# Performance work log

Measured on AMD Instinct MI355X. Metric: run time of the kernel, lower is better.

Reference implementation:

```python
import jax, jax.numpy as jnp
import numpy as np

GRID = (192, 96, 192)
NUM_MATERIALS = 8
WORLD_SCALE = 2.0
OCC_THRESHOLD = 0.01
TEMPERATURE = 1.0


def _look_at(eye, target, up):
    eye = np.asarray(eye, np.float32); target = np.asarray(target, np.float32); up = np.asarray(up, np.float32)
    f = target - eye; f = f / np.linalg.norm(f)
    r = np.cross(f, up); r = r / np.linalg.norm(r)
    u = np.cross(r, f)
    view = np.eye(4, dtype=np.float32)
    view[0, :3] = r;  view[0, 3] = -r @ eye
    view[1, :3] = u;  view[1, 3] = -u @ eye
    view[2, :3] = -f; view[2, 3] = f @ eye
    return view


def _perspective(fov_deg, aspect, near, far):
    f = 1.0 / np.tan(np.radians(fov_deg) / 2.0)
    p = np.zeros((4, 4), dtype=np.float32)
    p[0, 0] = f / aspect
    p[1, 1] = f
    p[2, 2] = (far + near) / (near - far)
    p[2, 3] = 2.0 * far * near / (near - far)
    p[3, 2] = -1.0
    return p


def setup_inputs() -> dict:
    key = jax.random.key(0)
    k1, k2 = jax.random.split(key)
    X, Y, Z = GRID
    occupancy_logits = jax.random.normal(k1, (X, Y, Z), dtype=jnp.float32)
    material_logits = jax.random.normal(k2, (X, Y, Z, NUM_MATERIALS), dtype=jnp.float32)
    # grid world extent: x,z in [-X/2, X/2]*scale, y in [0, Y]*scale
    camera_view = jnp.asarray(_look_at(eye=(0.0, 250.0, 700.0), target=(0.0, 96.0, 0.0), up=(0.0, 1.0, 0.0)))
    camera_proj = jnp.asarray(_perspective(60.0, 1.0, 0.1, 2000.0))
    return {
        'occupancy_logits': occupancy_logits,
        'material_logits': material_logits,
        'camera_view': camera_view,
        'camera_proj': camera_proj,
        'max_blocks': 100000,
    }


def _voxel_centers(X, Y, Z):
    # centers = (idx + 0.5 + offset) * world_scale, offset = (-X/2, 0, -Z/2)
    cx = (jnp.arange(X, dtype=jnp.float32) + 0.5 - X / 2.0) * WORLD_SCALE
    cy = (jnp.arange(Y, dtype=jnp.float32) + 0.5) * WORLD_SCALE
    cz = (jnp.arange(Z, dtype=jnp.float32) + 0.5 - Z / 2.0) * WORLD_SCALE
    gx, gy, gz = jnp.meshgrid(cx, cy, cz, indexing='ij')
    return jnp.stack([gx.ravel(), gy.ravel(), gz.ravel()], axis=-1)  # (N, 3)


def reference(occupancy_logits, material_logits, camera_view, camera_proj, max_blocks):
    X, Y, Z = occupancy_logits.shape
    N = X * Y * Z
    occ = jax.nn.sigmoid(occupancy_logits).reshape(-1)          # (N,)
    active = occ > OCC_THRESHOLD                                # torch.nonzero -> mask

    centers = _voxel_centers(X, Y, Z)                           # (N, 3) world centers

    # frustum test in NDC (world_to_clip with combined MVP)
    mvp = camera_proj @ camera_view                             # (4, 4)
    clip = centers @ mvp[:, :3].T + mvp[:, 3]                   # (N, 4)
    w = jnp.maximum(clip[:, 3], 1e-6)
    ndc = clip[:, :3] / w[:, None]
    visible = jnp.all((ndc >= -1.0) & (ndc <= 1.0), axis=-1)

    valid = active & visible

    # depth-based top-k: keep max_blocks nearest valid voxels
    view_z = centers @ camera_view[2, :3] + camera_view[2, 3]
    depth = jnp.maximum(-view_z, 0.0)
    score = jnp.where(valid, -depth, -jnp.inf)                  # nearest first
    _, idx = jax.lax.top_k(score, max_blocks)
    keep = jnp.zeros((N,), dtype=bool).at[idx].set(valid[idx])  # pruned_mask scatter

    pruned_weights = jnp.where(keep, occ, 0.0).reshape(X, Y, Z)

    # render prep: per-voxel material distribution scaled by occupancy weight
    mat_probs = jax.nn.softmax(material_logits / TEMPERATURE, axis=-1)
    return pruned_weights[..., None] * mat_probs                # (X, Y, Z, M)
```

## Files before the change

kernel.cpp:

```cpp
#include <hip/hip_runtime.h>

#define GX 192
#define GY 96
#define GZ 192
#define GRP (GY*GZ)
#define NVOX (GX*GRP)

#define NXC 12
#define XCW (GX/NXC)
#define GBLK (GRP/256)

#define K2T 1024
#define GPT (GRP/K2T)
#define WBINS 4096
#define BPT (WBINS/K2T)

#define WS_MVP    0
#define WS_G16    64
#define WS_DEPTH  (WS_G16 + GRP*16)
#define WS_SEL    (WS_DEPTH + GRP*4)
#define WS_TLIST  (WS_SEL + 16)
#define WS_TPREF  (WS_TLIST + 1024)
#define WS_NTIED  (WS_TPREF + GX*4)

typedef float f4 __attribute__((ext_vector_type(4)));

#define BSUM(w) (((w) & 255u) + (((w) >> 8) & 255u) + (((w) >> 16) & 255u) + ((w) >> 24))

__device__ __forceinline__ bool voxel_valid(int x, int g,
                                            const float* __restrict__ occL,
                                            const float* M,
                                            float* occ_out)
{
    int y = g / GZ;
    int z = g - y * GZ;
    float cx = (float)(2 * x - 191);
    float cy = (float)(2 * y + 1);
    float cz = (float)(2 * z - 191);

    float logit = occL[(size_t)x * GRP + g];
    float occ = 1.0f / (1.0f + expf(-logit));
    *occ_out = occ;
    if (!(occ > 0.01f)) return false;

    float c0 = __fadd_rn(__fmaf_rn(cz, M[2],  __fmaf_rn(cy, M[1],  __fmul_rn(cx, M[0]))),  M[3]);
    float c1 = __fadd_rn(__fmaf_rn(cz, M[6],  __fmaf_rn(cy, M[5],  __fmul_rn(cx, M[4]))),  M[7]);
    float c2 = __fadd_rn(__fmaf_rn(cz, M[10], __fmaf_rn(cy, M[9],  __fmul_rn(cx, M[8]))),  M[11]);
    float c3 = __fadd_rn(__fmaf_rn(cz, M[14], __fmaf_rn(cy, M[13], __fmul_rn(cx, M[12]))), M[15]);

    float w  = fmaxf(c3, 1e-6f);
    float nx = c0 / w;
    float ny = c1 / w;
    float nz = c2 / w;
    return (nx >= -1.0f) && (nx <= 1.0f) &&
           (ny >= -1.0f) && (ny <= 1.0f) &&
           (nz >= -1.0f) && (nz <= 1.0f);
}

__device__ __forceinline__ void compute_mvp_lds(const float* view, const float* proj,
                                                float* s_mvp, int tid)
{
    if (tid < 16) {
        int r = tid >> 2, c = tid & 3;
        float acc = 0.0f;
        for (int k = 0; k < 4; ++k)
            acc = __fadd_rn(acc, __fmul_rn(proj[r * 4 + k], view[k * 4 + c]));
        s_mvp[tid] = acc;
    }
}

__device__ __forceinline__ unsigned wave_incl_scan(unsigned v, int lane)
{
    #pragma unroll
    for (int off = 1; off < 64; off <<= 1) {
        unsigned u = (unsigned)__shfl_up((int)v, off);
        if (lane >= off) v += u;
    }
    return v;
}

__global__ __launch_bounds__(256) void k_prep_count(
    const float* __restrict__ view, const float* __restrict__ proj,
    const float* __restrict__ occL,
    float* __restrict__ mvpOut,
    unsigned char* __restrict__ g16,
    unsigned* __restrict__ depthBits)
{
    __shared__ float s_mvp[16];
    int tid = threadIdx.x;
    compute_mvp_lds(view, proj, s_mvp, tid);
    __syncthreads();

    int b  = blockIdx.x;
    int gb = b % GBLK;
    int xc = b / GBLK;
    int g  = gb * 256 + tid;

    if (b == 0 && tid < 16) mvpOut[tid] = s_mvp[tid];

    if (xc == 0) {
        int y = g / GZ;
        int z = g - y * GZ;
        float cy = (float)(2 * y + 1);
        float cz = (float)(2 * z - 191);
        float seed = __fmul_rn(-191.0f, view[8]);
        float vz = __fadd_rn(__fmaf_rn(cz, view[10], __fmaf_rn(cy, view[9], seed)), view[11]);
        float d  = fmaxf(-vz, 0.0f);
        unsigned db = __float_as_uint(d);
        __builtin_nontemporal_store(db, (unsigned*)(g16 + (size_t)g * 16));
        __builtin_nontemporal_store(db, &depthBits[g]);
    }

    unsigned c = 0;
    int x0 = xc * XCW;
    #pragma unroll
    for (int j = 0; j < XCW; ++j) {
        float occ;
        if (voxel_valid(x0 + j, g, occL, s_mvp, &occ)) ++c;
    }
    __builtin_nontemporal_store((unsigned char)c, g16 + (size_t)g * 16 + 4 + xc);
}

__global__ __launch_bounds__(1024) void k_select(
    const float* __restrict__ view, const float* __restrict__ proj,
    const float* __restrict__ occL,
    const unsigned char* __restrict__ g16,
    const int* __restrict__ maxBlocksPtr,
    unsigned* __restrict__ sel,
    unsigned* __restrict__ tiedList,
    unsigned* __restrict__ tiedPrefX,
    unsigned* __restrict__ nTiedG)
{
    __shared__ float s_mvp[16];
    __shared__ unsigned s_h[WBINS];
    __shared__ unsigned s_w[16];
    __shared__ unsigned s_wT[16], s_wMn[16], s_wMx[16];
    __shared__ unsigned s_tot, s_mn, s_mx, s_chTot;
    __shared__ unsigned s_found, s_prefix, s_remK;
    __shared__ unsigned s_list[256];
    __shared__ int s_n;
    __shared__ unsigned s_cntX[GX];

    int tid  = threadIdx.x;
    int lane = tid & 63;
    int wid  = tid >> 6;
    compute_mvp_lds(view, proj, s_mvp, tid);

    uint4 q[GPT];
    #pragma unroll
    for (int k = 0; k < GPT; ++k)
        q[k] = *(const uint4*)(g16 + (size_t)(tid + k * K2T) * 16);

    unsigned d[GPT], c[GPT];
    #pragma unroll
    for (int k = 0; k < GPT; ++k) {
        d[k] = q[k].x;
        c[k] = BSUM(q[k].y) + BSUM(q[k].z) + BSUM(q[k].w);
    }

    unsigned tot = 0, mn = 0xFFFFFFFFu, mx = 0;
    #pragma unroll
    for (int k = 0; k < GPT; ++k) {
        tot += c[k];
        if (c[k]) {
            unsigned hi = d[k] >> 16;
            mn = min(mn, hi);
            mx = max(mx, hi);
        }
    }
    for (int m = 1; m < 64; m <<= 1) {
        tot += (unsigned)__shfl_xor((int)tot, m);
        mn = min(mn, (unsigned)__shfl_xor((int)mn, m));
        mx = max(mx, (unsigned)__shfl_xor((int)mx, m));
    }
    if (lane == 0) { s_wT[wid] = tot; s_wMn[wid] = mn; s_wMx[wid] = mx; }
    __syncthreads();
    if (tid == 0) {
        unsigned t2 = 0, m2 = 0xFFFFFFFFu, x2 = 0;
        for (int w = 0; w < 16; ++w) {
            t2 += s_wT[w]; m2 = min(m2, s_wMn[w]); x2 = max(x2, s_wMx[w]);
        }
        s_tot = t2; s_mn = m2; s_mx = x2;
        s_found = 0;
    }
    __syncthreads();
    unsigned K = (unsigned)maxBlocksPtr[0];
    tot = s_tot; mn = s_mn; mx = s_mx;

    if (tot <= K) {
        if (tid == 0) {
            sel[0] = 0xFFFFFFFFu;
            sel[1] = 0x7FFFFFFFu;
            *nTiedG = 0u;
        }
        return;
    }

    unsigned remK = K;
    unsigned prefix = 0;
    unsigned span = mx - mn + 1u;
    unsigned nchunks = (span + WBINS - 1u) / WBINS;
    for (unsigned ch = 0; ch < nchunks; ++ch) {
        unsigned base = mn + ch * WBINS;
        #pragma unroll
        for (int j = 0; j < BPT; ++j) s_h[tid + j * K2T] = 0;
        __syncthreads();
        #pragma unroll
        for (int k = 0; k < GPT; ++k) {
            if (c[k]) {
                unsigned hi = d[k] >> 16;
                if (hi >= base && hi < base + WBINS)
                    atomicAdd(&s_h[hi - base], c[k]);
            }
        }
        __syncthreads();
        unsigned ps = 0;
        #pragma unroll
        for (int j = 0; j < BPT; ++j) ps += s_h[tid * BPT + j];
        unsigned iw = wave_incl_scan(ps, lane);
        if (lane == 63) s_w[wid] = iw;
        __syncthreads();
        if (wid == 0) {
            unsigned wv = (lane < 16) ? s_w[lane] : 0u;
            unsigned wiw = wave_incl_scan(wv, lane);
            if (lane < 16) s_w[lane] = wiw - wv;
            if (lane == 15) s_chTot = wiw;
        }
        __syncthreads();
        unsigned incl = iw + s_w[wid];
        unsigned chunkTot = s_chTot;
        unsigned excl = incl - ps;
        if (remK <= chunkTot && excl < remK && remK <= incl) {
            unsigned cum = excl;
            #pragma unroll
            for (int j = 0; j < BPT; ++j) {
                unsigned hv = s_h[tid * BPT + j];
                if (cum < remK && remK <= cum + hv) {
                    s_found  = 1u;
                    s_prefix = base + (unsigned)(tid * BPT + j);
                    s_remK   = remK - cum;
                }
                cum += hv;
            }
        }
        __syncthreads();
        if (s_found) { prefix = s_prefix; remK = s_remK; break; }
        remK -= chunkTot;
        __syncthreads();
    }

    for (int p = 0; p < 2; ++p) {
        int matchShift = (p == 0) ? 16 : 8;
        int digitShift = (p == 0) ? 8 : 0;
        if (tid < 256) s_h[tid] = 0;
        __syncthreads();
        #pragma unroll
        for (int k = 0; k < GPT; ++k) {
            if (c[k] && (d[k] >> matchShift) == prefix)
                atomicAdd(&s_h[(d[k] >> digitShift) & 255u], c[k]);
        }
        __syncthreads();
        unsigned ps = (tid < 256) ? s_h[tid] : 0u;
        unsigned iw = wave_incl_scan(ps, lane);
        if (lane == 63) s_w[wid] = iw;
        __syncthreads();
        if (wid == 0) {
            unsigned wv = (lane < 16) ? s_w[lane] : 0u;
            unsigned wiw = wave_incl_scan(wv, lane);
            if (lane < 16) s_w[lane] = wiw - wv;
        }
        __syncthreads();
        unsigned incl = iw + s_w[wid];
        unsigned excl = incl - ps;
        if (excl < remK && remK <= incl) {
            s_prefix = (prefix << 8) | (unsigned)tid;
            s_remK   = remK - excl;
        }
        __syncthreads();
        prefix = s_prefix; remK = s_remK;
        __syncthreads();
    }
    unsigned T = prefix;
    unsigned R = remK;

    if (tid == 0) s_n = 0;
    for (int x = tid; x < GX; x += K2T) s_cntX[x] = 0;
    __syncthreads();
    #pragma unroll
    for (int k = 0; k < GPT; ++k) {
        if (d[k] == T) {
            int idx = atomicAdd(&s_n, 1);
            if (idx < 256) s_list[idx] = (unsigned)(tid + k * K2T);
        }
    }
    __syncthreads();
    int n = min(s_n, 256);
    if (tid == 0) {
        for (int a = 1; a < n; ++a) {
            unsigned v = s_list[a];
            int b = a - 1;
            while (b >= 0 && s_list[b] > v) { s_list[b + 1] = s_list[b]; --b; }
            s_list[b + 1] = v;
        }
    }
    __syncthreads();
    int pairs = GX * n;
    for (int pr = tid; pr < pairs; pr += K2T) {
        int x = pr / n;
        int s = pr - x * n;
        float occ;
        if (voxel_valid(x, (int)s_list[s], occL, s_mvp, &occ))
            atomicAdd(&s_cntX[x], 1u);
    }
    __syncthreads();
    if (tid == 0) {
        unsigned run = 0;
        for (int x = 0; x < GX; ++x) { tiedPrefX[x] = run; run += s_cntX[x]; }
        *nTiedG = (unsigned)n;
        sel[0] = T;
        sel[1] = R;
    }
    if (tid < n) tiedList[tid] = s_list[tid];
}

__global__ __launch_bounds__(256) void k_out(
    const float* __restrict__ occL,
    const float* __restrict__ matL,
    const float* __restrict__ mvp,
    const unsigned* __restrict__ depthBits,
    const unsigned* __restrict__ sel,
    const unsigned* __restrict__ tiedList,
    const unsigned* __restrict__ tiedPrefX,
    const unsigned* __restrict__ nTiedPtr,
    float* __restrict__ out)
{
    int i = blockIdx.x * 256 + threadIdx.x;
    if (i >= NVOX) return;
    int x = i / GRP;
    int g = i - x * GRP;

    float occ;
    bool valid = voxel_valid(x, g, occL, mvp, &occ);
    bool keep = false;
    if (valid) {
        unsigned T  = sel[0];
        unsigned db = depthBits[g];
        if (db < T) {
            keep = true;
        } else if (db == T) {
            unsigned R = sel[1];
            unsigned rank = tiedPrefX[x];
            int n = (int)*nTiedPtr;
            for (int s = 0; s < n; ++s) {
                unsigned gs = tiedList[s];
                if (gs >= (unsigned)g) break;
                float o2;
                if (voxel_valid(x, (int)gs, occL, mvp, &o2)) ++rank;
            }
            keep = rank < R;
        }
    }

    f4 o0 = (f4)(0.0f);
    f4 o1 = (f4)(0.0f);
    if (keep) {
        const f4* mp = reinterpret_cast<const f4*>(matL) + (size_t)i * 2;
        f4 a = __builtin_nontemporal_load(mp);
        f4 b = __builtin_nontemporal_load(mp + 1);
        float mx = fmaxf(fmaxf(fmaxf(a[0], a[1]), fmaxf(a[2], a[3])),
                         fmaxf(fmaxf(b[0], b[1]), fmaxf(b[2], b[3])));
        float e0 = expf(a[0] - mx), e1 = expf(a[1] - mx), e2 = expf(a[2] - mx), e3 = expf(a[3] - mx);
        float e4 = expf(b[0] - mx), e5 = expf(b[1] - mx), e6 = expf(b[2] - mx), e7 = expf(b[3] - mx);
        float s = ((e0 + e1) + (e2 + e3)) + ((e4 + e5) + (e6 + e7));
        float inv = occ / s;
        o0[0] = e0 * inv; o0[1] = e1 * inv; o0[2] = e2 * inv; o0[3] = e3 * inv;
        o1[0] = e4 * inv; o1[1] = e5 * inv; o1[2] = e6 * inv; o1[3] = e7 * inv;
    }
    f4* op = reinterpret_cast<f4*>(out) + (size_t)i * 2;
    __builtin_nontemporal_store(o0, op);
    __builtin_nontemporal_store(o1, op + 1);
}

extern "C" void kernel_launch(void* const* d_in, const int* in_sizes, int n_in,
                              void* d_out, int out_size, void* d_ws, size_t ws_size,
                              hipStream_t stream)
{
    const float* occL = (const float*)d_in[0];
    const float* matL = (const float*)d_in[1];
    const float* view = (const float*)d_in[2];
    const float* proj = (const float*)d_in[3];
    const int*   mb   = (const int*)d_in[4];

    char* ws = (char*)d_ws;
    float*          mvp      = (float*)(ws + WS_MVP);
    unsigned char*  g16      = (unsigned char*)(ws + WS_G16);
    unsigned*       depthB   = (unsigned*)(ws + WS_DEPTH);
    unsigned*       sel      = (unsigned*)(ws + WS_SEL);
    unsigned*       tiedList = (unsigned*)(ws + WS_TLIST);
    unsigned*       tiedPref = (unsigned*)(ws + WS_TPREF);
    unsigned*       nTied    = (unsigned*)(ws + WS_NTIED);

    k_prep_count<<<NXC * GBLK, 256, 0, stream>>>(view, proj, occL, mvp, g16, depthB);
    k_select<<<1, K2T, 0, stream>>>(view, proj, occL, g16, mb,
                                    sel, tiedList, tiedPref, nTied);
    k_out<<<NVOX / 256, 256, 0, stream>>>(occL, matL, mvp, depthB, sel,
                                          tiedList, tiedPref, nTied, (float*)d_out);
}
```

Before: 66.79 us.

## Split selection into multi-block count reduction with last-block radix select

Replaces the single 1024-thread selection kernel with a 72-block kernel. Each block sums the per-group voxel counts into a byte array, and the last block to finish (detected with an atomic counter) runs a four-pass 8-bit radix select over recomputed depth bits. Dropping the wide chunked histogram is meant to shorten the serial single-block phase and spread the initial g16 reads across many CUs. In exchange the last block does 72 strided passes per radix round with only 256 threads, and a device-wide atomic plus threadfence handshake is added.

```diff
diff --git a/kernel.cpp b/kernel.cpp
--- a/kernel.cpp
+++ b/kernel.cpp
@@ -10,15 +10,15 @@
 #define XCW (GX/NXC)
 #define GBLK (GRP/256)
 
-#define K2T 1024
-#define GPT (GRP/K2T)
-#define WBINS 4096
-#define BPT (WBINS/K2T)
+#define SB   (GRP/256)
+#define SGPT (GRP/256)
 
 #define WS_MVP    0
 #define WS_G16    64
-#define WS_DEPTH  (WS_G16 + GRP*16)
-#define WS_SEL    (WS_DEPTH + GRP*4)
+#define WS_DEPTH  (WS_G16 + (size_t)GRP*16)
+#define WS_CSUM   (WS_DEPTH + GRP*4)
+#define WS_DONE   (WS_CSUM + GRP)
+#define WS_SEL    (WS_DONE + 16)
 #define WS_TLIST  (WS_SEL + 16)
 #define WS_TPREF  (WS_TLIST + 1024)
 #define WS_NTIED  (WS_TPREF + GX*4)
@@ -57,6 +57,18 @@
            (nz >= -1.0f) && (nz <= 1.0f);
 }
 
+__device__ __forceinline__ unsigned depth_bits(int g, float v8, float v9,
+                                               float v10, float v11)
+{
+    int y = g / GZ;
+    int z = g - y * GZ;
+    float cy = (float)(2 * y + 1);
+    float cz = (float)(2 * z - 191);
+    float seed = __fmul_rn(-191.0f, v8);
+    float vz = __fadd_rn(__fmaf_rn(cz, v10, __fmaf_rn(cy, v9, seed)), v11);
+    return __float_as_uint(fmaxf(-vz, 0.0f));
+}
+
 __device__ __forceinline__ void compute_mvp_lds(const float* view, const float* proj,
                                                 float* s_mvp, int tid)
 {
@@ -84,7 +96,8 @@
     const float* __restrict__ occL,
     float* __restrict__ mvpOut,
     unsigned char* __restrict__ g16,
-    unsigned* __restrict__ depthBits)
+    unsigned* __restrict__ depthBits,
+    unsigned* __restrict__ doneCnt)
 {
     __shared__ float s_mvp[16];
     int tid = threadIdx.x;
@@ -96,20 +109,13 @@
     int xc = b / GBLK;
     int g  = gb * 256 + tid;
 
-    if (b == 0 && tid < 16) mvpOut[tid] = s_mvp[tid];
-
-    if (xc == 0) {
-        int y = g / GZ;
-        int z = g - y * GZ;
-        float cy = (float)(2 * y + 1);
-        float cz = (float)(2 * z - 191);
-        float seed = __fmul_rn(-191.0f, view[8]);
-        float vz = __fadd_rn(__fmaf_rn(cz, view[10], __fmaf_rn(cy, view[9], seed)), view[11]);
-        float d  = fmaxf(-vz, 0.0f);
-        unsigned db = __float_as_uint(d);
-        __builtin_nontemporal_store(db, (unsigned*)(g16 + (size_t)g * 16));
-        __builtin_nontemporal_store(db, &depthBits[g]);
-    }
+    if (b == 0) {
+        if (tid < 16) mvpOut[tid] = s_mvp[tid];
+        if (tid == 0) *doneCnt = 0u;
+    }
+
+    if (xc == 0)
+        depthBits[g] = depth_bits(g, view[8], view[9], view[10], view[11]);
 
     unsigned c = 0;
     int x0 = xc * XCW;
@@ -118,160 +124,90 @@
         float occ;
         if (voxel_valid(x0 + j, g, occL, s_mvp, &occ)) ++c;
     }
-    __builtin_nontemporal_store((unsigned char)c, g16 + (size_t)g * 16 + 4 + xc);
-}
-
-__global__ __launch_bounds__(1024) void k_select(
+    g16[(size_t)g * 16 + 4 + xc] = (unsigned char)c;
+}
+
+__global__ __launch_bounds__(256) void k_sumsel(
     const float* __restrict__ view, const float* __restrict__ proj,
     const float* __restrict__ occL,
     const unsigned char* __restrict__ g16,
+    unsigned char* __restrict__ cnt8sum,
+    unsigned* __restrict__ doneCnt,
     const int* __restrict__ maxBlocksPtr,
     unsigned* __restrict__ sel,
     unsigned* __restrict__ tiedList,
     unsigned* __restrict__ tiedPrefX,
     unsigned* __restrict__ nTiedG)
 {
+    __shared__ unsigned s_last;
     __shared__ float s_mvp[16];
-    __shared__ unsigned s_h[WBINS];
-    __shared__ unsigned s_w[16];
-    __shared__ unsigned s_wT[16], s_wMn[16], s_wMx[16];
-    __shared__ unsigned s_tot, s_mn, s_mx, s_chTot;
-    __shared__ unsigned s_found, s_prefix, s_remK;
+    __shared__ unsigned s_h[256];
+    __shared__ unsigned s_w[4];
+    __shared__ unsigned s_tot;
+    __shared__ unsigned s_prefix, s_remK;
     __shared__ unsigned s_list[256];
     __shared__ int s_n;
     __shared__ unsigned s_cntX[GX];
 
-    int tid  = threadIdx.x;
+    int tid = threadIdx.x;
+    int g0  = blockIdx.x * 256 + tid;
+
+    uint4 q = *(const uint4*)(g16 + (size_t)g0 * 16);
+    cnt8sum[g0] = (unsigned char)(BSUM(q.y) + BSUM(q.z) + BSUM(q.w));
+
+    __threadfence();
+    if (tid == 0) {
+        unsigned old = atomicAdd(doneCnt, 1u);
+        s_last = (old == SB - 1) ? 1u : 0u;
+    }
+    __syncthreads();
+    if (!s_last) return;
+    __threadfence();
+
+    compute_mvp_lds(view, proj, s_mvp, tid);
+    float v8 = view[8], v9 = view[9], v10 = view[10], v11 = view[11];
     int lane = tid & 63;
     int wid  = tid >> 6;
-    compute_mvp_lds(view, proj, s_mvp, tid);
-
-    uint4 q[GPT];
-    #pragma unroll
-    for (int k = 0; k < GPT; ++k)
-        q[k] = *(const uint4*)(g16 + (size_t)(tid + k * K2T) * 16);
-
-    unsigned d[GPT], c[GPT];
-    #pragma unroll
-    for (int k = 0; k < GPT; ++k) {
-        d[k] = q[k].x;
-        c[k] = BSUM(q[k].y) + BSUM(q[k].z) + BSUM(q[k].w);
-    }
-
-    unsigned tot = 0, mn = 0xFFFFFFFFu, mx = 0;
-    #pragma unroll
-    for (int k = 0; k < GPT; ++k) {
-        tot += c[k];
-        if (c[k]) {
-            unsigned hi = d[k] >> 16;
-            mn = min(mn, hi);
-            mx = max(mx, hi);
-        }
-    }
-    for (int m = 1; m < 64; m <<= 1) {
-        tot += (unsigned)__shfl_xor((int)tot, m);
-        mn = min(mn, (unsigned)__shfl_xor((int)mn, m));
-        mx = max(mx, (unsigned)__shfl_xor((int)mx, m));
-    }
-    if (lane == 0) { s_wT[wid] = tot; s_wMn[wid] = mn; s_wMx[wid] = mx; }
-    __syncthreads();
-    if (tid == 0) {
-        unsigned t2 = 0, m2 = 0xFFFFFFFFu, x2 = 0;
-        for (int w = 0; w < 16; ++w) {
-            t2 += s_wT[w]; m2 = min(m2, s_wMn[w]); x2 = max(x2, s_wMx[w]);
-        }
-        s_tot = t2; s_mn = m2; s_mx = x2;
-        s_found = 0;
-    }
-    __syncthreads();
     unsigned K = (unsigned)maxBlocksPtr[0];
-    tot = s_tot; mn = s_mn; mx = s_mx;
-
-    if (tot <= K) {
-        if (tid == 0) {
-            sel[0] = 0xFFFFFFFFu;
-            sel[1] = 0x7FFFFFFFu;
-            *nTiedG = 0u;
-        }
-        return;
-    }
-
-    unsigned remK = K;
-    unsigned prefix = 0;
-    unsigned span = mx - mn + 1u;
-    unsigned nchunks = (span + WBINS - 1u) / WBINS;
-    for (unsigned ch = 0; ch < nchunks; ++ch) {
-        unsigned base = mn + ch * WBINS;
-        #pragma unroll
-        for (int j = 0; j < BPT; ++j) s_h[tid + j * K2T] = 0;
-        __syncthreads();
-        #pragma unroll
-        for (int k = 0; k < GPT; ++k) {
-            if (c[k]) {
-                unsigned hi = d[k] >> 16;
-                if (hi >= base && hi < base + WBINS)
-                    atomicAdd(&s_h[hi - base], c[k]);
-            }
-        }
-        __syncthreads();
-        unsigned ps = 0;
-        #pragma unroll
-        for (int j = 0; j < BPT; ++j) ps += s_h[tid * BPT + j];
+
+    unsigned prefix = 0, remK = K;
+    for (int p = 0; p < 4; ++p) {
+        int shift = 24 - 8 * p;
+        s_h[tid] = 0;
+        __syncthreads();
+        for (int j = 0; j < SGPT; ++j) {
+            int g = tid + j * 256;
+            unsigned cc = cnt8sum[g];
+            if (!cc) continue;
+            unsigned db = depth_bits(g, v8, v9, v10, v11);
+            if (p > 0 && (db >> (shift + 8)) != prefix) continue;
+            atomicAdd(&s_h[(db >> shift) & 255u], cc);
+        }
+        __syncthreads();
+        unsigned ps = s_h[tid];
         unsigned iw = wave_incl_scan(ps, lane);
         if (lane == 63) s_w[wid] = iw;
         __syncthreads();
         if (wid == 0) {
-            unsigned wv = (lane < 16) ? s_w[lane] : 0u;
+            unsigned wv = (lane < 4) ? s_w[lane] : 0u;
             unsigned wiw = wave_incl_scan(wv, lane);
-            if (lane < 16) s_w[lane] = wiw - wv;
-            if (lane == 15) s_chTot = wiw;
-        }
-        __syncthreads();
-        unsigned incl = iw + s_w[wid];
-        unsigned chunkTot = s_chTot;
-        unsigned excl = incl - ps;
-        if (remK <= chunkTot && excl < remK && remK <= incl) {
-            unsigned cum = excl;
-            #pragma unroll
-            for (int j = 0; j < BPT; ++j) {
-                unsigned hv = s_h[tid * BPT + j];
-                if (cum < remK && remK <= cum + hv) {
-                    s_found  = 1u;
-                    s_prefix = base + (unsigned)(tid * BPT + j);
-                    s_remK   = remK - cum;
-                }
-                cum += hv;
-            }
-        }
-        __syncthreads();
-        if (s_found) { prefix = s_prefix; remK = s_remK; break; }
-        remK -= chunkTot;
-        __syncthreads();
-    }
-
-    for (int p = 0; p < 2; ++p) {
-        int matchShift = (p == 0) ? 16 : 8;
-        int digitShift = (p == 0) ? 8 : 0;
-        if (tid < 256) s_h[tid] = 0;
-        __syncthreads();
-        #pragma unroll
-        for (int k = 0; k < GPT; ++k) {
-            if (c[k] && (d[k] >> matchShift) == prefix)
-                atomicAdd(&s_h[(d[k] >> digitShift) & 255u], c[k]);
-        }
-        __syncthreads();
-        unsigned ps = (tid < 256) ? s_h[tid] : 0u;
-        unsigned iw = wave_incl_scan(ps, lane);
-        if (lane == 63) s_w[wid] = iw;
-        __syncthreads();
-        if (wid == 0) {
-            unsigned wv = (lane < 16) ? s_w[lane] : 0u;
-            unsigned wiw = wave_incl_scan(wv, lane);
-            if (lane < 16) s_w[lane] = wiw - wv;
+            if (lane < 4) s_w[lane] = wiw - wv;
+            if (lane == 3) s_tot = wiw;
         }
         __syncthreads();
         unsigned incl = iw + s_w[wid];
         unsigned excl = incl - ps;
+
+        if (p == 0) {
+            if (s_tot <= K) {
+                if (tid == 0) {
+                    sel[0] = 0xFFFFFFFFu;
+                    sel[1] = 0x7FFFFFFFu;
+                    *nTiedG = 0u;
+                }
+                return;
+            }
+        }
         if (excl < remK && remK <= incl) {
             s_prefix = (prefix << 8) | (unsigned)tid;
             s_remK   = remK - excl;
@@ -284,13 +220,13 @@
     unsigned R = remK;
 
     if (tid == 0) s_n = 0;
-    for (int x = tid; x < GX; x += K2T) s_cntX[x] = 0;
-    __syncthreads();
-    #pragma unroll
-    for (int k = 0; k < GPT; ++k) {
-        if (d[k] == T) {
+    if (tid < GX) s_cntX[tid] = 0;
+    __syncthreads();
+    for (int j = 0; j < SGPT; ++j) {
+        int g = tid + j * 256;
+        if (depth_bits(g, v8, v9, v10, v11) == T) {
             int idx = atomicAdd(&s_n, 1);
-            if (idx < 256) s_list[idx] = (unsigned)(tid + k * K2T);
+            if (idx < 256) s_list[idx] = (unsigned)g;
         }
     }
     __syncthreads();
@@ -298,14 +234,14 @@
     if (tid == 0) {
         for (int a = 1; a < n; ++a) {
             unsigned v = s_list[a];
-            int b = a - 1;
-            while (b >= 0 && s_list[b] > v) { s_list[b + 1] = s_list[b]; --b; }
-            s_list[b + 1] = v;
+            int b2 = a - 1;
+            while (b2 >= 0 && s_list[b2] > v) { s_list[b2 + 1] = s_list[b2]; --b2; }
+            s_list[b2 + 1] = v;
         }
     }
     __syncthreads();
     int pairs = GX * n;
-    for (int pr = tid; pr < pairs; pr += K2T) {
+    for (int pr = tid; pr < pairs; pr += 256) {
         int x = pr / n;
         int s = pr - x * n;
         float occ;
@@ -395,14 +331,16 @@
     float*          mvp      = (float*)(ws + WS_MVP);
     unsigned char*  g16      = (unsigned char*)(ws + WS_G16);
     unsigned*       depthB   = (unsigned*)(ws + WS_DEPTH);
+    unsigned char*  csum     = (unsigned char*)(ws + WS_CSUM);
+    unsigned*       done     = (unsigned*)(ws + WS_DONE);
     unsigned*       sel      = (unsigned*)(ws + WS_SEL);
     unsigned*       tiedList = (unsigned*)(ws + WS_TLIST);
     unsigned*       tiedPref = (unsigned*)(ws + WS_TPREF);
     unsigned*       nTied    = (unsigned*)(ws + WS_NTIED);
 
-    k_prep_count<<<NXC * GBLK, 256, 0, stream>>>(view, proj, occL, mvp, g16, depthB);
-    k_select<<<1, K2T, 0, stream>>>(view, proj, occL, g16, mb,
-                                    sel, tiedList, tiedPref, nTied);
+    k_prep_count<<<NXC * GBLK, 256, 0, stream>>>(view, proj, occL, mvp, g16, depthB, done);
+    k_sumsel<<<SB, 256, 0, stream>>>(view, proj, occL, g16, csum, done, mb,
+                                     sel, tiedList, tiedPref, nTied);
     k_out<<<NVOX / 256, 256, 0, stream>>>(occL, matL, mvp, depthB, sel,
                                           tiedList, tiedPref, nTied, (float*)d_out);
 }
```

Result: slower. 114.0 us (+70.7%).
